# Kernel tuning notes

Hardware: AMD Instinct MI355X
Metric: run time of the kernel (lower is better)

The kernel has to match this reference:

```python
import jax, jax.numpy as jnp
import numpy as np

EPS = 1e-10
COMMITMENT_COST = 0.25


def setup_inputs() -> dict:
    key = jax.random.key(0)
    k1, k2 = jax.random.split(key)
    inputs = jax.random.normal(k1, (64, 64, 32, 32), dtype=jnp.float32)
    # nn.init.uniform_(weight, -1.0, 1.0)
    embeddings = jax.random.uniform(k2, (1024, 64), dtype=jnp.float32, minval=-1.0, maxval=1.0)
    return {"inputs": inputs, "embeddings": embeddings}


def reference(inputs, embeddings):
    B, C, H, W = inputs.shape  # C == embedding_dim
    K = embeddings.shape[0]
    x = jnp.transpose(inputs, (0, 2, 3, 1)).reshape(-1, C)  # [N, D]
    d = (jnp.sum(x * x, axis=1, keepdims=True)
         - 2.0 * (x @ embeddings.T)
         + jnp.sum(embeddings * embeddings, axis=1))  # [N, K]
    idx = jnp.argmin(d, axis=1)  # [N]
    # one-hot @ embeddings == gather
    q = jnp.take(embeddings, idx, axis=0)  # [N, D]
    x4 = x.reshape(B, H, W, C)
    q4 = q.reshape(B, H, W, C)
    e_latent = jnp.mean((jax.lax.stop_gradient(q4) - x4) ** 2)
    q_latent = jnp.mean((q4 - jax.lax.stop_gradient(x4)) ** 2)
    loss = q_latent + COMMITMENT_COST * e_latent
    # straight-through estimator
    st = x4 + jax.lax.stop_gradient(q4 - x4)
    # avg_probs = mean of one-hot encodings == normalized histogram
    n = idx.shape[0]
    avg_probs = jnp.zeros((K,), dtype=jnp.float32).at[idx].add(1.0) / n
    perplexity = jnp.exp(-jnp.sum(avg_probs * jnp.log(avg_probs + EPS)))
    quantized = jnp.transpose(st, (0, 3, 1, 2))
    return quantized, loss, perplexity
```

## Files before the change

### kernel.cpp

```cpp
#include <hip/hip_runtime.h>

#define N_TOTAL   65536
#define HW_SZ     1024
#define CDIM      64
#define K_CODES   1024
#define OUT_ELEMS 4194304
#define QT        256
#define NCHUNK    4
#define TAU       0.004f


typedef __attribute__((ext_vector_type(8))) short short8;
typedef __attribute__((ext_vector_type(4))) float f32x4;

__device__ __forceinline__ unsigned short f2bf(float x) {
    unsigned u = __float_as_uint(x);
    return (unsigned short)((u + 0x7FFFu + ((u >> 16) & 1u)) >> 16);
}
__device__ __forceinline__ float bf2f(unsigned short h) {
    return __uint_as_float(((unsigned)h) << 16);
}
__device__ __forceinline__ void gload_lds16(const void* g, void* l) {
    __builtin_amdgcn_global_load_lds(
        (const __attribute__((address_space(1))) void*)g,
        (__attribute__((address_space(3))) void*)l, 16, 0, 0);
}

__global__ void k_prep(const float* __restrict__ emb, float* __restrict__ enorm,
                       short* __restrict__ btab, unsigned int* __restrict__ hist) {
    int gid = blockIdx.x * 256 + threadIdx.x;
    int r  = gid >> 4;
    int d0 = (gid & 15) * 4;
    float4 v = *(const float4*)(emb + gid * 4);
    float s = v.x * v.x + v.y * v.y + v.z * v.z + v.w * v.w;
#pragma unroll
    for (int off = 1; off < 16; off <<= 1) s += __shfl_xor(s, off, 64);
    if ((gid & 15) == 0) enorm[r] = s;

    float vv[4] = {v.x, v.y, v.z, v.w};
    short h[4], l[4];
#pragma unroll
    for (int j = 0; j < 4; ++j) {
        unsigned short hh = f2bf(vv[j]);
        h[j] = (short)hh;
        l[j] = (short)f2bf(vv[j] - bf2f(hh));
    }
    int base = (r >> 4) * 2048 + (d0 >> 5) * 1024
             + ((((d0 >> 3) & 3) * 16 + (r & 15)) * 8) + (d0 & 7);
    *(short4*)&btab[base]       = make_short4(h[0], h[1], h[2], h[3]);
    *(short4*)&btab[base + 512] = make_short4(l[0], l[1], l[2], l[3]);

    if (gid < K_CODES) hist[gid] = 0u;
}

__global__ __launch_bounds__(512, 2)
void k_argmin(const float* __restrict__ x, const float* __restrict__ emb,
              const short* __restrict__ btab, const float* __restrict__ enorm,
              unsigned int* __restrict__ hist, float* __restrict__ partials,
              float* __restrict__ out) {
    __shared__ __align__(16) short bufs[2][16 * 2048];
    __shared__ __align__(16) float ens[K_CODES];
    __shared__ float xnorm[QT];
    __shared__ float rd1[QT];
    __shared__ float rd2[QT];
    __shared__ int   ri[QT];
    __shared__ int   flist[QT];
    __shared__ __align__(16) float xqf[CDIM];
    __shared__ float wdd[8];
    __shared__ int   wii[8];
    __shared__ float spw[4];
    __shared__ int   nflag;
    float* tile = (float*)bufs;

    const int tid  = threadIdx.x;
    const int lane = tid & 63;
    const int w    = tid >> 6;
    const int quad = lane >> 4;
    const int col  = lane & 15;

    const int n0  = blockIdx.x * QT;
    const int b   = n0 >> 10;
    const int hw0 = n0 & 1023;

    auto stage_async = [&](int c, int bsel) {
        const short* src = btab + c * (16 * 2048);
#pragma unroll
        for (int i = 0; i < 8; ++i) {
            int idx = i * 512 + tid;
            gload_lds16(&src[idx * 8], (void*)&bufs[bsel][idx * 8]);
        }
    };

    stage_async(0, 0);
    if (tid < 256) gload_lds16(&enorm[tid * 4], (void*)&ens[tid * 4]);

    const float* xb = x + b * (CDIM * HW_SZ) + hw0 + col;
    short8 afr[2][2][2];
#pragma unroll
    for (int rt = 0; rt < 2; ++rt) {
        float nloc = 0.f;
#pragma unroll
        for (int kc = 0; kc < 2; ++kc) {
#pragma unroll
            for (int j = 0; j < 8; ++j) {
                int c0 = (kc * 4 + quad) * 8 + j;
                float v = xb[c0 * HW_SZ + w * 32 + rt * 16];
                unsigned short hh = f2bf(v);
                afr[rt][kc][0][j] = (short)hh;
                afr[rt][kc][1][j] = (short)f2bf(v - bf2f(hh));
                nloc = __builtin_fmaf(v, v, nloc);
            }
        }
        nloc += __shfl_xor(nloc, 16, 64);
        nloc += __shfl_xor(nloc, 32, 64);
        if (quad == 0) xnorm[w * 32 + rt * 16 + col] = nloc;
    }

    float d1[8], d2[8];
    int   i1[8];
#pragma unroll
    for (int t = 0; t < 8; ++t) { d1[t] = 3.4e38f; d2[t] = 3.4e38f; i1[t] = 0; }

    __syncthreads();

    for (int c = 0; c < NCHUNK; ++c) {
        if (c + 1 < NCHUNK) stage_async(c + 1, (c + 1) & 1);
        const short* bs = &bufs[c & 1][0];
        const int cbase = c * 256;

        short8 Ba[4], Bb[4];
        float  ena, enb;
        auto LDB = [&](short8 (&B)[4], float& en, int ctl) {
            const short* fp = bs + ctl * 2048 + lane * 8;
            B[0] = *(const short8*)(fp);
            B[1] = *(const short8*)(fp + 512);
            B[2] = *(const short8*)(fp + 1024);
            B[3] = *(const short8*)(fp + 1536);
            en   = ens[cbase + ctl * 16 + col];
        };
        auto COMP = [&](const short8 (&B)[4], float en, int mycode) {
#pragma unroll
            for (int rt = 0; rt < 2; ++rt) {
                f32x4 a0 = {0.f, 0.f, 0.f, 0.f};
                f32x4 a1 = {0.f, 0.f, 0.f, 0.f};
                a0 = __builtin_amdgcn_mfma_f32_16x16x32_bf16(afr[rt][0][1], B[0], a0, 0, 0, 0);
                a1 = __builtin_amdgcn_mfma_f32_16x16x32_bf16(afr[rt][1][1], B[2], a1, 0, 0, 0);
                a0 = __builtin_amdgcn_mfma_f32_16x16x32_bf16(afr[rt][0][0], B[1], a0, 0, 0, 0);
                a1 = __builtin_amdgcn_mfma_f32_16x16x32_bf16(afr[rt][1][0], B[3], a1, 0, 0, 0);
                a0 = __builtin_amdgcn_mfma_f32_16x16x32_bf16(afr[rt][0][0], B[0], a0, 0, 0, 0);
                a1 = __builtin_amdgcn_mfma_f32_16x16x32_bf16(afr[rt][1][0], B[2], a1, 0, 0, 0);
#pragma unroll
                for (int reg = 0; reg < 4; ++reg) {
                    int t = rt * 4 + reg;
                    float dot = a0[reg] + a1[reg];
                    float d   = __builtin_fmaf(dot, -2.f, en);
                    float d1o = d1[t];
                    d2[t] = __builtin_amdgcn_fmed3f(d, d1o, d2[t]);
                    d1[t] = fminf(d, d1o);
                    i1[t] = (d < d1o) ? mycode : i1[t];
                }
            }
        };

        LDB(Ba, ena, 0);
#pragma unroll
        for (int ctl = 0; ctl < 16; ctl += 2) {
            LDB(Bb, enb, ctl + 1);
            COMP(Ba, ena, cbase + ctl * 16 + col);
            if (ctl + 2 < 16) LDB(Ba, ena, ctl + 2);
            COMP(Bb, enb, cbase + (ctl + 1) * 16 + col);
        }
        __syncthreads();
    }

#pragma unroll
    for (int t = 0; t < 8; ++t) {
        float a1 = d1[t], a2 = d2[t];
        int ai = i1[t];
#pragma unroll
        for (int off = 1; off < 16; off <<= 1) {
            float o1 = __shfl_xor(a1, off, 64);
            float o2 = __shfl_xor(a2, off, 64);
            int   oi = __shfl_xor(ai, off, 64);
            if (o1 < a1 || (o1 == a1 && oi < ai)) {
                float loser = a1; a2 = fminf(fminf(a2, o2), loser); a1 = o1; ai = oi;
            } else {
                a2 = fminf(fminf(a2, o2), o1);
            }
        }
        d1[t] = a1; d2[t] = a2; i1[t] = ai;
    }

    if (tid == 0) nflag = 0;
    if (col == 0) {
#pragma unroll
        for (int rt = 0; rt < 2; ++rt)
#pragma unroll
            for (int reg = 0; reg < 4; ++reg) {
                int t = rt * 4 + reg;
                int m = w * 32 + rt * 16 + quad * 4 + reg;
                rd1[m] = d1[t];
                rd2[m] = d2[t];
                ri [m] = i1[t];
            }
    }
    __syncthreads();

    if (tid < QT) {
        if (rd2[tid] - rd1[tid] < TAU) {
            int slot = atomicAdd(&nflag, 1);
            flist[slot] = tid;
        }
    }
    __syncthreads();

    for (int f = 0; f < nflag; ++f) {
        const int q = flist[f];
        if (tid < CDIM) xqf[tid] = x[b * (CDIM * HW_SZ) + tid * HW_SZ + hw0 + q];
        __syncthreads();
        float dm = 3.4e38f; int im = 0;
#pragma unroll
        for (int cd = 0; cd < 2; ++cd) {
            const int k = tid + cd * 512;
            const float4* er = (const float4*)(emb + k * CDIM);
            const float4* xr = (const float4*)xqf;
            float dot = 0.f;
#pragma unroll
            for (int c4 = 0; c4 < 16; ++c4) {
                float4 e = er[c4], xv = xr[c4];
                dot += e.x * xv.x + e.y * xv.y + e.z * xv.z + e.w * xv.w;
            }
            float d = ens[k] - 2.f * dot;
            if (d < dm) { dm = d; im = k; }
        }
#pragma unroll
        for (int off = 1; off < 64; off <<= 1) {
            float od = __shfl_xor(dm, off, 64);
            int   oi = __shfl_xor(im, off, 64);
            if (od < dm || (od == dm && oi < im)) { dm = od; im = oi; }
        }
        if (lane == 0) { wdd[w] = dm; wii[w] = im; }
        __syncthreads();
        if (tid == 0) {
            float bd = wdd[0]; int bi = wii[0];
#pragma unroll
            for (int ww = 1; ww < 8; ++ww)
                if (wdd[ww] < bd || (wdd[ww] == bd && wii[ww] < bi)) { bd = wdd[ww]; bi = wii[ww]; }
            rd1[q] = bd; ri[q] = bi;
        }
        __syncthreads();
    }

    if (tid < QT) {
        int ai = ri[tid];
        atomicAdd(&hist[ai], 1u);
        float sp = rd1[tid] + xnorm[tid];
#pragma unroll
        for (int off = 32; off; off >>= 1) sp += __shfl_down(sp, off, 64);
        if (lane == 0) spw[w] = sp;
    }
    __syncthreads();
    if (tid == 0) partials[blockIdx.x] = spw[0] + spw[1] + spw[2] + spw[3];

#pragma unroll
    for (int h = 0; h < 4; ++h) {
        {
            int q = tid >> 3, j8 = tid & 7;
            int code = ri[h * 64 + q];
            int ct = code >> 4, cl = code & 15;
            int kc = j8 >> 2, qd = j8 & 3;
            const short* tb = btab + ct * 2048 + kc * 1024;
            short8 hi = *(const short8*)&tb[(qd * 16 + cl) * 8];
            short8 lo = *(const short8*)&tb[512 + (qd * 16 + cl) * 8];
            float* dst = &tile[q * 72 + j8 * 8];
#pragma unroll
            for (int k = 0; k < 8; ++k)
                dst[k] = bf2f((unsigned short)hi[k]) + bf2f((unsigned short)lo[k]);
        }
        __syncthreads();
        {
            int c = tid >> 3;
            float* ob = out + b * (CDIM * HW_SZ) + c * HW_SZ + hw0 + h * 64;
#pragma unroll
            for (int p = 0; p < 2; ++p) {
                int q = ((tid & 7) + p * 8) * 4;
                float4 v;
                v.x = tile[(q + 0) * 72 + c];
                v.y = tile[(q + 1) * 72 + c];
                v.z = tile[(q + 2) * 72 + c];
                v.w = tile[(q + 3) * 72 + c];
                *(float4*)&ob[q] = v;
            }
        }
        if (h < 3) __syncthreads();
    }
}

__global__ void k_final(const float* __restrict__ partials,
                        const unsigned int* __restrict__ hist,
                        float* __restrict__ out) {
    int tid = threadIdx.x;
    float ss = partials[tid];
    float s = 0.f;
#pragma unroll
    for (int i = 0; i < 4; ++i) {
        float p = (float)hist[i * 256 + tid] * (1.0f / 65536.0f);
        s += p * logf(p + 1e-10f);
    }
    __shared__ float fin[8];
#pragma unroll
    for (int off = 32; off; off >>= 1) {
        ss += __shfl_down(ss, off, 64);
        s  += __shfl_down(s, off, 64);
    }
    if ((tid & 63) == 0) { fin[tid >> 6] = ss; fin[4 + (tid >> 6)] = s; }
    __syncthreads();
    if (tid == 0) {
        float sse = fin[0] + fin[1] + fin[2] + fin[3];
        float ent = fin[4] + fin[5] + fin[6] + fin[7];
        out[OUT_ELEMS]     = 1.25f * sse * (1.0f / (float)OUT_ELEMS);
        out[OUT_ELEMS + 1] = expf(-ent);
    }
}

extern "C" void kernel_launch(void* const* d_in, const int* in_sizes, int n_in,
                              void* d_out, int out_size, void* d_ws, size_t ws_size,
                              hipStream_t stream) {
    const float* x   = (const float*)d_in[0];
    const float* emb = (const float*)d_in[1];
    float* out = (float*)d_out;
    char* ws = (char*)d_ws;
    float*        enorm    = (float*)(ws);
    unsigned int* hist     = (unsigned int*)(ws + 4096);
    float*        partials = (float*)(ws + 8192);
    short*        btab     = (short*)(ws + 12288);

    k_prep  <<<64, 256, 0, stream>>>(emb, enorm, btab, hist);
    k_argmin<<<N_TOTAL / QT, 512, 0, stream>>>(x, emb, btab, enorm, hist, partials, out);
    k_final <<<1, 256, 0, stream>>>(partials, hist, out);
}
```

Before: 124.2 us.

## Split argmin epilogue into separate kernel with smaller blocks

```diff
diff --git a/kernel.cpp b/kernel.cpp
--- a/kernel.cpp
+++ b/kernel.cpp
@@ -6,6 +6,7 @@
 #define K_CODES   1024
 #define OUT_ELEMS 4194304
 #define QT        256
+#define QB        128
 #define NCHUNK    4
 #define TAU       0.004f
 
@@ -54,23 +55,16 @@
 }
 
 __global__ __launch_bounds__(512, 2)
-void k_argmin(const float* __restrict__ x, const float* __restrict__ emb,
-              const short* __restrict__ btab, const float* __restrict__ enorm,
-              unsigned int* __restrict__ hist, float* __restrict__ partials,
-              float* __restrict__ out) {
+void k_argmin(const float* __restrict__ x, const short* __restrict__ btab,
+              const float* __restrict__ enorm,
+              float* __restrict__ rd1g, float* __restrict__ rd2g,
+              int* __restrict__ rig, float* __restrict__ xng) {
     __shared__ __align__(16) short bufs[2][16 * 2048];
     __shared__ __align__(16) float ens[K_CODES];
     __shared__ float xnorm[QT];
     __shared__ float rd1[QT];
     __shared__ float rd2[QT];
     __shared__ int   ri[QT];
-    __shared__ int   flist[QT];
-    __shared__ __align__(16) float xqf[CDIM];
-    __shared__ float wdd[8];
-    __shared__ int   wii[8];
-    __shared__ float spw[4];
-    __shared__ int   nflag;
-    float* tile = (float*)bufs;
 
     const int tid  = threadIdx.x;
     const int lane = tid & 63;
@@ -191,7 +185,6 @@
         d1[t] = a1; d2[t] = a2; i1[t] = ai;
     }
 
-    if (tid == 0) nflag = 0;
     if (col == 0) {
 #pragma unroll
         for (int rt = 0; rt < 2; ++rt)
@@ -207,6 +200,52 @@
     __syncthreads();
 
     if (tid < QT) {
+        rd1g[n0 + tid] = rd1[tid];
+        rd2g[n0 + tid] = rd2[tid];
+        rig [n0 + tid] = ri[tid];
+        xng [n0 + tid] = xnorm[tid];
+    }
+}
+
+__global__ __launch_bounds__(256, 4)
+void k_epi(const float* __restrict__ x, const float* __restrict__ emb,
+           const float* __restrict__ enorm,
+           const float* __restrict__ rd1g, const float* __restrict__ rd2g,
+           const int* __restrict__ rig, const float* __restrict__ xng,
+           unsigned int* __restrict__ hist, float* __restrict__ partials,
+           float* __restrict__ out) {
+    __shared__ __align__(16) float ens[K_CODES];
+    __shared__ float rd1[QB];
+    __shared__ float rd2[QB];
+    __shared__ int   ri[QB];
+    __shared__ float xn[QB];
+    __shared__ int   flist[QB];
+    __shared__ __align__(16) float xqf[CDIM];
+    __shared__ float wdd[4];
+    __shared__ int   wii[4];
+    __shared__ float spw[2];
+    __shared__ int   nflag;
+    __shared__ __align__(16) float tile[64 * 72];
+
+    const int tid  = threadIdx.x;
+    const int lane = tid & 63;
+    const int w    = tid >> 6;
+
+    const int n0  = blockIdx.x * QB;
+    const int b   = n0 >> 10;
+    const int hw0 = n0 & 1023;
+
+    gload_lds16(&enorm[tid * 4], (void*)&ens[tid * 4]);
+    if (tid == 0) nflag = 0;
+    if (tid < QB) {
+        rd1[tid] = rd1g[n0 + tid];
+        rd2[tid] = rd2g[n0 + tid];
+        ri [tid] = rig [n0 + tid];
+        xn [tid] = xng [n0 + tid];
+    }
+    __syncthreads();
+
+    if (tid < QB) {
         if (rd2[tid] - rd1[tid] < TAU) {
             int slot = atomicAdd(&nflag, 1);
             flist[slot] = tid;
@@ -220,8 +259,8 @@
         __syncthreads();
         float dm = 3.4e38f; int im = 0;
 #pragma unroll
-        for (int cd = 0; cd < 2; ++cd) {
-            const int k = tid + cd * 512;
+        for (int cd = 0; cd < 4; ++cd) {
+            const int k = tid + cd * 256;
             const float4* er = (const float4*)(emb + k * CDIM);
             const float4* xr = (const float4*)xqf;
             float dot = 0.f;
@@ -244,46 +283,44 @@
         if (tid == 0) {
             float bd = wdd[0]; int bi = wii[0];
 #pragma unroll
-            for (int ww = 1; ww < 8; ++ww)
+            for (int ww = 1; ww < 4; ++ww)
                 if (wdd[ww] < bd || (wdd[ww] == bd && wii[ww] < bi)) { bd = wdd[ww]; bi = wii[ww]; }
             rd1[q] = bd; ri[q] = bi;
         }
         __syncthreads();
     }
 
-    if (tid < QT) {
+    if (tid < QB) {
         int ai = ri[tid];
         atomicAdd(&hist[ai], 1u);
-        float sp = rd1[tid] + xnorm[tid];
+        float sp = rd1[tid] + xn[tid];
 #pragma unroll
         for (int off = 32; off; off >>= 1) sp += __shfl_down(sp, off, 64);
         if (lane == 0) spw[w] = sp;
     }
     __syncthreads();
-    if (tid == 0) partials[blockIdx.x] = spw[0] + spw[1] + spw[2] + spw[3];
-
-#pragma unroll
-    for (int h = 0; h < 4; ++h) {
+    if (tid == 0) partials[blockIdx.x] = spw[0] + spw[1];
+
+#pragma unroll
+    for (int h = 0; h < 2; ++h) {
         {
-            int q = tid >> 3, j8 = tid & 7;
+            int q = tid >> 2, j = tid & 3;
             int code = ri[h * 64 + q];
-            int ct = code >> 4, cl = code & 15;
-            int kc = j8 >> 2, qd = j8 & 3;
-            const short* tb = btab + ct * 2048 + kc * 1024;
-            short8 hi = *(const short8*)&tb[(qd * 16 + cl) * 8];
-            short8 lo = *(const short8*)&tb[512 + (qd * 16 + cl) * 8];
-            float* dst = &tile[q * 72 + j8 * 8];
-#pragma unroll
-            for (int k = 0; k < 8; ++k)
-                dst[k] = bf2f((unsigned short)hi[k]) + bf2f((unsigned short)lo[k]);
+            const float4* er = (const float4*)(emb + code * CDIM + j * 16);
+            float4 e0 = er[0], e1 = er[1], e2 = er[2], e3 = er[3];
+            float* dst = &tile[q * 72 + j * 16];
+            *(float4*)&dst[0]  = e0;
+            *(float4*)&dst[4]  = e1;
+            *(float4*)&dst[8]  = e2;
+            *(float4*)&dst[12] = e3;
         }
         __syncthreads();
         {
-            int c = tid >> 3;
+            int c = tid >> 2;
             float* ob = out + b * (CDIM * HW_SZ) + c * HW_SZ + hw0 + h * 64;
 #pragma unroll
-            for (int p = 0; p < 2; ++p) {
-                int q = ((tid & 7) + p * 8) * 4;
+            for (int p = 0; p < 4; ++p) {
+                int q = ((tid & 3) + p * 4) * 4;
                 float4 v;
                 v.x = tile[(q + 0) * 72 + c];
                 v.y = tile[(q + 1) * 72 + c];
@@ -292,7 +329,7 @@
                 *(float4*)&ob[q] = v;
             }
         }
-        if (h < 3) __syncthreads();
+        if (h == 0) __syncthreads();
     }
 }
 
@@ -300,7 +337,7 @@
                         const unsigned int* __restrict__ hist,
                         float* __restrict__ out) {
     int tid = threadIdx.x;
-    float ss = partials[tid];
+    float ss = partials[tid] + partials[256 + tid];
     float s = 0.f;
 #pragma unroll
     for (int i = 0; i < 4; ++i) {
@@ -334,8 +371,14 @@
     unsigned int* hist     = (unsigned int*)(ws + 4096);
     float*        partials = (float*)(ws + 8192);
     short*        btab     = (short*)(ws + 12288);
+    float*        rd1g     = (float*)(ws + 274432);
+    float*        rd2g     = (float*)(ws + 536576);
+    int*          rig      = (int*)  (ws + 798720);
+    float*        xng      = (float*)(ws + 1060864);
 
     k_prep  <<<64, 256, 0, stream>>>(emb, enorm, btab, hist);
-    k_argmin<<<N_TOTAL / QT, 512, 0, stream>>>(x, emb, btab, enorm, hist, partials, out);
+    k_argmin<<<N_TOTAL / QT, 512, 0, stream>>>(x, btab, enorm, rd1g, rd2g, rig, xng);
+    k_epi   <<<N_TOTAL / QB, 256, 0, stream>>>(x, emb, enorm, rd1g, rd2g, rig, xng,
+                                               hist, partials, out);
     k_final <<<1, 256, 0, stream>>>(partials, hist, out);
 }
```

New measurement: 169.6 us. 36.5% more time.

## Move histogram to final kernel via LDS atomics and gather fp32 codewords directly

Applied to the files above, without the earlier changes.

```diff
diff --git a/kernel.cpp b/kernel.cpp
--- a/kernel.cpp
+++ b/kernel.cpp
@@ -27,7 +27,7 @@
 }
 
 __global__ void k_prep(const float* __restrict__ emb, float* __restrict__ enorm,
-                       short* __restrict__ btab, unsigned int* __restrict__ hist) {
+                       short* __restrict__ btab) {
     int gid = blockIdx.x * 256 + threadIdx.x;
     int r  = gid >> 4;
     int d0 = (gid & 15) * 4;
@@ -49,14 +49,12 @@
              + ((((d0 >> 3) & 3) * 16 + (r & 15)) * 8) + (d0 & 7);
     *(short4*)&btab[base]       = make_short4(h[0], h[1], h[2], h[3]);
     *(short4*)&btab[base + 512] = make_short4(l[0], l[1], l[2], l[3]);
-
-    if (gid < K_CODES) hist[gid] = 0u;
 }
 
 __global__ __launch_bounds__(512, 2)
 void k_argmin(const float* __restrict__ x, const float* __restrict__ emb,
               const short* __restrict__ btab, const float* __restrict__ enorm,
-              unsigned int* __restrict__ hist, float* __restrict__ partials,
+              int* __restrict__ rig, float* __restrict__ partials,
               float* __restrict__ out) {
     __shared__ __align__(16) short bufs[2][16 * 2048];
     __shared__ __align__(16) float ens[K_CODES];
@@ -219,13 +217,12 @@
         if (tid < CDIM) xqf[tid] = x[b * (CDIM * HW_SZ) + tid * HW_SZ + hw0 + q];
         __syncthreads();
         float dm = 3.4e38f; int im = 0;
-#pragma unroll
         for (int cd = 0; cd < 2; ++cd) {
             const int k = tid + cd * 512;
             const float4* er = (const float4*)(emb + k * CDIM);
             const float4* xr = (const float4*)xqf;
             float dot = 0.f;
-#pragma unroll
+#pragma unroll 4
             for (int c4 = 0; c4 < 16; ++c4) {
                 float4 e = er[c4], xv = xr[c4];
                 dot += e.x * xv.x + e.y * xv.y + e.z * xv.z + e.w * xv.w;
@@ -252,8 +249,7 @@
     }
 
     if (tid < QT) {
-        int ai = ri[tid];
-        atomicAdd(&hist[ai], 1u);
+        rig[n0 + tid] = ri[tid];
         float sp = rd1[tid] + xnorm[tid];
 #pragma unroll
         for (int off = 32; off; off >>= 1) sp += __shfl_down(sp, off, 64);
@@ -267,15 +263,11 @@
         {
             int q = tid >> 3, j8 = tid & 7;
             int code = ri[h * 64 + q];
-            int ct = code >> 4, cl = code & 15;
-            int kc = j8 >> 2, qd = j8 & 3;
-            const short* tb = btab + ct * 2048 + kc * 1024;
-            short8 hi = *(const short8*)&tb[(qd * 16 + cl) * 8];
-            short8 lo = *(const short8*)&tb[512 + (qd * 16 + cl) * 8];
+            const float4* er = (const float4*)(emb + code * CDIM + j8 * 8);
+            float4 e0 = er[0], e1 = er[1];
             float* dst = &tile[q * 72 + j8 * 8];
-#pragma unroll
-            for (int k = 0; k < 8; ++k)
-                dst[k] = bf2f((unsigned short)hi[k]) + bf2f((unsigned short)lo[k]);
+            *(float4*)&dst[0] = e0;
+            *(float4*)&dst[4] = e1;
         }
         __syncthreads();
         {
@@ -296,28 +288,34 @@
     }
 }
 
-__global__ void k_final(const float* __restrict__ partials,
-                        const unsigned int* __restrict__ hist,
-                        float* __restrict__ out) {
+__global__ __launch_bounds__(1024, 1)
+void k_final(const int* __restrict__ rig, const float* __restrict__ partials,
+             float* __restrict__ out) {
+    __shared__ unsigned int lhist[K_CODES];
+    __shared__ float fin[32];
     int tid = threadIdx.x;
-    float ss = partials[tid];
-    float s = 0.f;
-#pragma unroll
-    for (int i = 0; i < 4; ++i) {
-        float p = (float)hist[i * 256 + tid] * (1.0f / 65536.0f);
-        s += p * logf(p + 1e-10f);
-    }
-    __shared__ float fin[8];
+
+    if (tid < K_CODES) lhist[tid] = 0u;
+    __syncthreads();
+#pragma unroll
+    for (int i = 0; i < N_TOTAL / 1024; ++i)
+        atomicAdd(&lhist[rig[i * 1024 + tid]], 1u);
+    __syncthreads();
+
+    float ss = (tid < 256) ? partials[tid] : 0.f;
+    float p  = (float)lhist[tid] * (1.0f / 65536.0f);
+    float s  = p * logf(p + 1e-10f);
 #pragma unroll
     for (int off = 32; off; off >>= 1) {
         ss += __shfl_down(ss, off, 64);
         s  += __shfl_down(s, off, 64);
     }
-    if ((tid & 63) == 0) { fin[tid >> 6] = ss; fin[4 + (tid >> 6)] = s; }
+    if ((tid & 63) == 0) { fin[tid >> 6] = ss; fin[16 + (tid >> 6)] = s; }
     __syncthreads();
     if (tid == 0) {
-        float sse = fin[0] + fin[1] + fin[2] + fin[3];
-        float ent = fin[4] + fin[5] + fin[6] + fin[7];
+        float sse = 0.f, ent = 0.f;
+#pragma unroll
+        for (int i = 0; i < 16; ++i) { sse += fin[i]; ent += fin[16 + i]; }
         out[OUT_ELEMS]     = 1.25f * sse * (1.0f / (float)OUT_ELEMS);
         out[OUT_ELEMS + 1] = expf(-ent);
     }
@@ -331,11 +329,11 @@
     float* out = (float*)d_out;
     char* ws = (char*)d_ws;
     float*        enorm    = (float*)(ws);
-    unsigned int* hist     = (unsigned int*)(ws + 4096);
     float*        partials = (float*)(ws + 8192);
     short*        btab     = (short*)(ws + 12288);
-
-    k_prep  <<<64, 256, 0, stream>>>(emb, enorm, btab, hist);
-    k_argmin<<<N_TOTAL / QT, 512, 0, stream>>>(x, emb, btab, enorm, hist, partials, out);
-    k_final <<<1, 256, 0, stream>>>(partials, hist, out);
-}
+    int*          rig      = (int*)  (ws + 274432);
+
+    k_prep  <<<64, 256, 0, stream>>>(emb, enorm, btab);
+    k_argmin<<<N_TOTAL / QT, 512, 0, stream>>>(x, emb, btab, enorm, rig, partials, out);
+    k_final <<<1, 1024, 0, stream>>>(rig, partials, out);
+}
```

Result: slower. 154.0 us (+24.0%).

## Use 1024-thread blocks with one row tile per wave in argmin kernel

Applied to the files above, without the earlier changes.

```diff
diff --git a/kernel.cpp b/kernel.cpp
--- a/kernel.cpp
+++ b/kernel.cpp
@@ -53,7 +53,7 @@
     if (gid < K_CODES) hist[gid] = 0u;
 }
 
-__global__ __launch_bounds__(512, 2)
+__global__ __launch_bounds__(1024, 1)
 void k_argmin(const float* __restrict__ x, const float* __restrict__ emb,
               const short* __restrict__ btab, const float* __restrict__ enorm,
               unsigned int* __restrict__ hist, float* __restrict__ partials,
@@ -66,8 +66,8 @@
     __shared__ int   ri[QT];
     __shared__ int   flist[QT];
     __shared__ __align__(16) float xqf[CDIM];
-    __shared__ float wdd[8];
-    __shared__ int   wii[8];
+    __shared__ float wdd[16];
+    __shared__ int   wii[16];
     __shared__ float spw[4];
     __shared__ int   nflag;
     float* tile = (float*)bufs;
@@ -85,8 +85,8 @@
     auto stage_async = [&](int c, int bsel) {
         const short* src = btab + c * (16 * 2048);
 #pragma unroll
-        for (int i = 0; i < 8; ++i) {
-            int idx = i * 512 + tid;
+        for (int i = 0; i < 4; ++i) {
+            int idx = i * 1024 + tid;
             gload_lds16(&src[idx * 8], (void*)&bufs[bsel][idx * 8]);
         }
     };
@@ -94,32 +94,29 @@
     stage_async(0, 0);
     if (tid < 256) gload_lds16(&enorm[tid * 4], (void*)&ens[tid * 4]);
 
-    const float* xb = x + b * (CDIM * HW_SZ) + hw0 + col;
-    short8 afr[2][2][2];
-#pragma unroll
-    for (int rt = 0; rt < 2; ++rt) {
-        float nloc = 0.f;
-#pragma unroll
-        for (int kc = 0; kc < 2; ++kc) {
-#pragma unroll
-            for (int j = 0; j < 8; ++j) {
-                int c0 = (kc * 4 + quad) * 8 + j;
-                float v = xb[c0 * HW_SZ + w * 32 + rt * 16];
-                unsigned short hh = f2bf(v);
-                afr[rt][kc][0][j] = (short)hh;
-                afr[rt][kc][1][j] = (short)f2bf(v - bf2f(hh));
-                nloc = __builtin_fmaf(v, v, nloc);
-            }
-        }
-        nloc += __shfl_xor(nloc, 16, 64);
-        nloc += __shfl_xor(nloc, 32, 64);
-        if (quad == 0) xnorm[w * 32 + rt * 16 + col] = nloc;
-    }
-
-    float d1[8], d2[8];
-    int   i1[8];
-#pragma unroll
-    for (int t = 0; t < 8; ++t) { d1[t] = 3.4e38f; d2[t] = 3.4e38f; i1[t] = 0; }
+    const float* xb = x + b * (CDIM * HW_SZ) + hw0 + w * 16 + col;
+    short8 afr[2][2];
+    float nloc = 0.f;
+#pragma unroll
+    for (int kc = 0; kc < 2; ++kc) {
+#pragma unroll
+        for (int j = 0; j < 8; ++j) {
+            int c0 = (kc * 4 + quad) * 8 + j;
+            float v = xb[c0 * HW_SZ];
+            unsigned short hh = f2bf(v);
+            afr[kc][0][j] = (short)hh;
+            afr[kc][1][j] = (short)f2bf(v - bf2f(hh));
+            nloc = __builtin_fmaf(v, v, nloc);
+        }
+    }
+    nloc += __shfl_xor(nloc, 16, 64);
+    nloc += __shfl_xor(nloc, 32, 64);
+    if (quad == 0) xnorm[w * 16 + col] = nloc;
+
+    float d1[4], d2[4];
+    int   i1[4];
+#pragma unroll
+    for (int t = 0; t < 4; ++t) { d1[t] = 3.4e38f; d2[t] = 3.4e38f; i1[t] = 0; }
 
     __syncthreads();
 
@@ -139,26 +136,22 @@
             en   = ens[cbase + ctl * 16 + col];
         };
         auto COMP = [&](const short8 (&B)[4], float en, int mycode) {
-#pragma unroll
-            for (int rt = 0; rt < 2; ++rt) {
-                f32x4 a0 = {0.f, 0.f, 0.f, 0.f};
-                f32x4 a1 = {0.f, 0.f, 0.f, 0.f};
-                a0 = __builtin_amdgcn_mfma_f32_16x16x32_bf16(afr[rt][0][1], B[0], a0, 0, 0, 0);
-                a1 = __builtin_amdgcn_mfma_f32_16x16x32_bf16(afr[rt][1][1], B[2], a1, 0, 0, 0);
-                a0 = __builtin_amdgcn_mfma_f32_16x16x32_bf16(afr[rt][0][0], B[1], a0, 0, 0, 0);
-                a1 = __builtin_amdgcn_mfma_f32_16x16x32_bf16(afr[rt][1][0], B[3], a1, 0, 0, 0);
-                a0 = __builtin_amdgcn_mfma_f32_16x16x32_bf16(afr[rt][0][0], B[0], a0, 0, 0, 0);
-                a1 = __builtin_amdgcn_mfma_f32_16x16x32_bf16(afr[rt][1][0], B[2], a1, 0, 0, 0);
-#pragma unroll
-                for (int reg = 0; reg < 4; ++reg) {
-                    int t = rt * 4 + reg;
-                    float dot = a0[reg] + a1[reg];
-                    float d   = __builtin_fmaf(dot, -2.f, en);
-                    float d1o = d1[t];
-                    d2[t] = __builtin_amdgcn_fmed3f(d, d1o, d2[t]);
-                    d1[t] = fminf(d, d1o);
-                    i1[t] = (d < d1o) ? mycode : i1[t];
-                }
+            f32x4 a0 = {0.f, 0.f, 0.f, 0.f};
+            f32x4 a1 = {0.f, 0.f, 0.f, 0.f};
+            a0 = __builtin_amdgcn_mfma_f32_16x16x32_bf16(afr[0][1], B[0], a0, 0, 0, 0);
+            a1 = __builtin_amdgcn_mfma_f32_16x16x32_bf16(afr[1][1], B[2], a1, 0, 0, 0);
+            a0 = __builtin_amdgcn_mfma_f32_16x16x32_bf16(afr[0][0], B[1], a0, 0, 0, 0);
+            a1 = __builtin_amdgcn_mfma_f32_16x16x32_bf16(afr[1][0], B[3], a1, 0, 0, 0);
+            a0 = __builtin_amdgcn_mfma_f32_16x16x32_bf16(afr[0][0], B[0], a0, 0, 0, 0);
+            a1 = __builtin_amdgcn_mfma_f32_16x16x32_bf16(afr[1][0], B[2], a1, 0, 0, 0);
+#pragma unroll
+            for (int reg = 0; reg < 4; ++reg) {
+                float dot = a0[reg] + a1[reg];
+                float d   = __builtin_fmaf(dot, -2.f, en);
+                float d1o = d1[reg];
+                d2[reg] = __builtin_amdgcn_fmed3f(d, d1o, d2[reg]);
+                d1[reg] = fminf(d, d1o);
+                i1[reg] = (d < d1o) ? mycode : i1[reg];
             }
         };
 
@@ -174,7 +167,7 @@
     }
 
 #pragma unroll
-    for (int t = 0; t < 8; ++t) {
+    for (int t = 0; t < 4; ++t) {
         float a1 = d1[t], a2 = d2[t];
         int ai = i1[t];
 #pragma unroll
@@ -194,15 +187,12 @@
     if (tid == 0) nflag = 0;
     if (col == 0) {
 #pragma unroll
-        for (int rt = 0; rt < 2; ++rt)
-#pragma unroll
-            for (int reg = 0; reg < 4; ++reg) {
-                int t = rt * 4 + reg;
-                int m = w * 32 + rt * 16 + quad * 4 + reg;
-                rd1[m] = d1[t];
-                rd2[m] = d2[t];
-                ri [m] = i1[t];
-            }
+        for (int reg = 0; reg < 4; ++reg) {
+            int m = w * 16 + quad * 4 + reg;
+            rd1[m] = d1[reg];
+            rd2[m] = d2[reg];
+            ri [m] = i1[reg];
+        }
     }
     __syncthreads();
 
@@ -218,21 +208,17 @@
         const int q = flist[f];
         if (tid < CDIM) xqf[tid] = x[b * (CDIM * HW_SZ) + tid * HW_SZ + hw0 + q];
         __syncthreads();
-        float dm = 3.4e38f; int im = 0;
-#pragma unroll
-        for (int cd = 0; cd < 2; ++cd) {
-            const int k = tid + cd * 512;
-            const float4* er = (const float4*)(emb + k * CDIM);
-            const float4* xr = (const float4*)xqf;
-            float dot = 0.f;
-#pragma unroll
-            for (int c4 = 0; c4 < 16; ++c4) {
-                float4 e = er[c4], xv = xr[c4];
-                dot += e.x * xv.x + e.y * xv.y + e.z * xv.z + e.w * xv.w;
-            }
-            float d = ens[k] - 2.f * dot;
-            if (d < dm) { dm = d; im = k; }
-        }
+        const int k = tid;
+        const float4* er = (const float4*)(emb + k * CDIM);
+        const float4* xr = (const float4*)xqf;
+        float dot = 0.f;
+#pragma unroll 4
+        for (int c4 = 0; c4 < 16; ++c4) {
+            float4 e = er[c4], xv = xr[c4];
+            dot += e.x * xv.x + e.y * xv.y + e.z * xv.z + e.w * xv.w;
+        }
+        float dm = ens[k] - 2.f * dot;
+        int   im = k;
 #pragma unroll
         for (int off = 1; off < 64; off <<= 1) {
             float od = __shfl_xor(dm, off, 64);
@@ -244,7 +230,7 @@
         if (tid == 0) {
             float bd = wdd[0]; int bi = wii[0];
 #pragma unroll
-            for (int ww = 1; ww < 8; ++ww)
+            for (int ww = 1; ww < 16; ++ww)
                 if (wdd[ww] < bd || (wdd[ww] == bd && wii[ww] < bi)) { bd = wdd[ww]; bi = wii[ww]; }
             rd1[q] = bd; ri[q] = bi;
         }
@@ -257,7 +243,7 @@
         float sp = rd1[tid] + xnorm[tid];
 #pragma unroll
         for (int off = 32; off; off >>= 1) sp += __shfl_down(sp, off, 64);
-        if (lane == 0) spw[w] = sp;
+        if (lane == 0) spw[tid >> 6] = sp;
     }
     __syncthreads();
     if (tid == 0) partials[blockIdx.x] = spw[0] + spw[1] + spw[2] + spw[3];
@@ -265,32 +251,21 @@
 #pragma unroll
     for (int h = 0; h < 4; ++h) {
         {
-            int q = tid >> 3, j8 = tid & 7;
+            int q = tid >> 4, j4 = tid & 15;
             int code = ri[h * 64 + q];
-            int ct = code >> 4, cl = code & 15;
-            int kc = j8 >> 2, qd = j8 & 3;
-            const short* tb = btab + ct * 2048 + kc * 1024;
-            short8 hi = *(const short8*)&tb[(qd * 16 + cl) * 8];
-            short8 lo = *(const short8*)&tb[512 + (qd * 16 + cl) * 8];
-            float* dst = &tile[q * 72 + j8 * 8];
-#pragma unroll
-            for (int k = 0; k < 8; ++k)
-                dst[k] = bf2f((unsigned short)hi[k]) + bf2f((unsigned short)lo[k]);
+            float4 e = *(const float4*)(emb + code * CDIM + j4 * 4);
+            *(float4*)&tile[q * 73 + j4 * 4] = e;
         }
         __syncthreads();
         {
-            int c = tid >> 3;
-            float* ob = out + b * (CDIM * HW_SZ) + c * HW_SZ + hw0 + h * 64;
-#pragma unroll
-            for (int p = 0; p < 2; ++p) {
-                int q = ((tid & 7) + p * 8) * 4;
-                float4 v;
-                v.x = tile[(q + 0) * 72 + c];
-                v.y = tile[(q + 1) * 72 + c];
-                v.z = tile[(q + 2) * 72 + c];
-                v.w = tile[(q + 3) * 72 + c];
-                *(float4*)&ob[q] = v;
-            }
+            int c = tid >> 4, s = tid & 15;
+            int q = s * 4;
+            float4 v;
+            v.x = tile[(q + 0) * 73 + c];
+            v.y = tile[(q + 1) * 73 + c];
+            v.z = tile[(q + 2) * 73 + c];
+            v.w = tile[(q + 3) * 73 + c];
+            *(float4*)&out[b * (CDIM * HW_SZ) + c * HW_SZ + hw0 + h * 64 + q] = v;
         }
         if (h < 3) __syncthreads();
     }
@@ -336,6 +311,6 @@
     short*        btab     = (short*)(ws + 12288);
 
     k_prep  <<<64, 256, 0, stream>>>(emb, enorm, btab, hist);
-    k_argmin<<<N_TOTAL / QT, 512, 0, stream>>>(x, emb, btab, enorm, hist, partials, out);
+    k_argmin<<<N_TOTAL / QT, 1024, 0, stream>>>(x, emb, btab, enorm, hist, partials, out);
     k_final <<<1, 256, 0, stream>>>(partials, hist, out);
 }
```

Result: slower. 153.9 us (+23.9%).
